# Kernel tuning notes

Measured on AMD Instinct MI355X. Metric: run time of the kernel, lower is better.

## Reference

```python
import jax, jax.numpy as jnp
import numpy as np

HIDDEN = 1024
STATE = 256
EXP = 4
LN_EPS = 1e-5


def setup_inputs() -> dict:
    key = jax.random.key(0)
    ks = jax.random.split(key, 10)
    B, T, H, S = 8, 2048, HIDDEN, STATE
    x = jax.random.normal(ks[0], (B, T, H), dtype=jnp.float32)
    A = jax.random.normal(ks[1], (S, S), dtype=jnp.float32) * 0.1
    Bm = jax.random.normal(ks[2], (S, H), dtype=jnp.float32) * 0.1
    C = jax.random.normal(ks[3], (H, S), dtype=jnp.float32) * 0.1
    D = jax.random.normal(ks[4], (H, H), dtype=jnp.float32) * 0.1
    ln_w = jnp.ones((H,), dtype=jnp.float32)
    ln_b = jnp.zeros((H,), dtype=jnp.float32)
    lim1 = 1.0 / np.sqrt(H)
    lim2 = 1.0 / np.sqrt(H * EXP)
    W1 = jax.random.uniform(ks[5], (H * EXP, H), minval=-lim1, maxval=lim1, dtype=jnp.float32)
    b1 = jax.random.uniform(ks[6], (H * EXP,), minval=-lim1, maxval=lim1, dtype=jnp.float32)
    W2 = jax.random.uniform(ks[7], (H, H * EXP), minval=-lim2, maxval=lim2, dtype=jnp.float32)
    b2 = jax.random.uniform(ks[8], (H,), minval=-lim2, maxval=lim2, dtype=jnp.float32)
    return {"x": x, "A": A, "Bm": Bm, "C": C, "D": D,
            "ln_w": ln_w, "ln_b": ln_b, "W1": W1, "b1": b1, "W2": W2, "b2": b2}


def _layernorm(y, w, b):
    mu = jnp.mean(y, axis=-1, keepdims=True)
    var = jnp.var(y, axis=-1, keepdims=True)
    return (y - mu) * jax.lax.rsqrt(var + LN_EPS) * w + b


def reference(x, A, Bm, C, D, ln_w, ln_b, W1, b1, W2, b2):
    Bsz, T, H = x.shape
    S = A.shape[0]
    state0 = jnp.zeros((Bsz, S), dtype=x.dtype)
    # Precompute input projections for all timesteps (big GEMMs outside the scan)
    xB = jnp.einsum('bth,sh->tbs', x, Bm)   # [T,B,S]
    xD = jnp.einsum('bth,oh->tbo', x, D)    # [T,B,H]

    def step(state, inp):
        xb_t, xd_t = inp
        state = jnp.tanh(state @ A.T + xb_t)
        out = state @ C.T + xd_t
        return state, out

    final_state, outs = jax.lax.scan(step, state0, (xB, xD))
    out_seq = jnp.transpose(outs, (1, 0, 2))  # [B,T,H]
    y = _layernorm(out_seq + x, ln_w, ln_b)
    # FFN (dropout is identity in eval mode); torch GELU default = exact erf
    h = jax.nn.gelu(jnp.einsum('bth,fh->btf', y, W1) + b1, approximate=False)
    y = y + jnp.einsum('btf,hf->bth', h, W2) + b2
    return (y, final_state)
```

## Files before the change

### kernel.cpp

```cpp
#include <hip/hip_runtime.h>
#include <math.h>

typedef unsigned short u16;
typedef unsigned int u32;

using short8 = __attribute__((ext_vector_type(8))) short;
using f32x4  = __attribute__((ext_vector_type(4))) float;
typedef _Float16 h2_t __attribute__((ext_vector_type(2)));

typedef const __attribute__((address_space(1))) unsigned int* gas_ptr;
typedef __attribute__((address_space(3))) unsigned int* las_ptr;

__device__ __forceinline__ void load_lds16(const void* g, void* l) {
    __builtin_amdgcn_global_load_lds((gas_ptr)g, (las_ptr)l, 16, 0, 0);
}

__device__ __forceinline__ u16 bf16b(float f) {
    u32 u = __builtin_bit_cast(u32, f);
    u += 0x7fffu + ((u >> 16) & 1u);
    return (u16)(u >> 16);
}
__device__ __forceinline__ float b2f(u16 h) {
    u32 u = (u32)h << 16;
    return __builtin_bit_cast(float, u);
}

__global__ void cvt_kernel(const float4* __restrict__ s, ushort4* __restrict__ d, int n4) {
    for (int i = blockIdx.x * blockDim.x + threadIdx.x; i < n4; i += gridDim.x * blockDim.x) {
        float4 v = s[i];
        ushort4 o;
        o.x = bf16b(v.x); o.y = bf16b(v.y); o.z = bf16b(v.z); o.w = bf16b(v.w);
        d[i] = o;
    }
}
__global__ void cvt_str_kernel(const float4* __restrict__ s, u16* __restrict__ d,
                               int K4, int n4, int stride, int col0) {
    for (int i = blockIdx.x * blockDim.x + threadIdx.x; i < n4; i += gridDim.x * blockDim.x) {
        float4 v = s[i];
        int r = i / K4, k4 = (i - r * K4) * 4;
        ushort4 o;
        o.x = bf16b(v.x); o.y = bf16b(v.y); o.z = bf16b(v.z); o.w = bf16b(v.w);
        *(ushort4*)(d + (size_t)r * stride + col0 + k4) = o;
    }
}

template<int MODE>
__global__ __launch_bounds__(256) void gemm_bf16(
    const u16* __restrict__ Ab, const u16* __restrict__ Ab2, const u16* __restrict__ Bb,
    int K, int ktiles,
    float* __restrict__ out32, u16* __restrict__ out16,
    const float* __restrict__ bias, const float* __restrict__ addf,
    const u16* __restrict__ add16, int out_stride)
{
    __shared__ __align__(16) u16 Als[128 * 64];
    __shared__ __align__(16) u16 Bls[128 * 64];

    const int tid  = threadIdx.x;
    const int lane = tid & 63;
    const int w    = tid >> 6;
    const int wr   = (w >> 1) * 64;
    const int wc   = (w & 1) * 64;
    const int fr   = lane & 15;
    const int fkB  = (lane >> 4) * 16;

    const size_t rbB = (size_t)K * 2;
    const int arow = blockIdx.y * 128 + (tid >> 3);
    const char* Ag  = (const char*)Ab + (size_t)arow * ((MODE == 1) ? 512 : rbB) + (size_t)(tid & 7) * 16;
    const char* Ag2 = (MODE == 1) ? ((const char*)Ab2 + (size_t)arow * 2048 + (size_t)(tid & 7) * 16) : nullptr;
    const char* Bg  = (const char*)Bb + ((size_t)blockIdx.x * 128 + (tid >> 3)) * rbB + (size_t)(tid & 7) * 16;
    char* Ald = (char*)Als + tid * 16;
    char* Bld = (char*)Bls + tid * 16;

    f32x4 acc[4][4];
#pragma unroll
    for (int m = 0; m < 4; ++m)
#pragma unroll
        for (int n = 0; n < 4; ++n)
            acc[m][n] = f32x4{0.f, 0.f, 0.f, 0.f};

    for (int kt = 0; kt < ktiles; ++kt) {
        __syncthreads();
        const char* Asrc;
        size_t rbA;
        if (MODE == 1) {
            if (kt < 4) { Asrc = Ag  + (size_t)kt * 128;       rbA = 512;  }
            else        { Asrc = Ag2 + (size_t)(kt - 4) * 128; rbA = 2048; }
        } else {
            Asrc = Ag + (size_t)kt * 128; rbA = rbB;
        }
        const char* Bsrc = Bg + (size_t)kt * 128;
#pragma unroll
        for (int i = 0; i < 4; ++i) {
            load_lds16(Asrc + (size_t)(i * 32) * rbA, Ald + i * 4096);
            load_lds16(Bsrc + (size_t)(i * 32) * rbB, Bld + i * 4096);
        }
        __syncthreads();
#pragma unroll
        for (int kk = 0; kk < 2; ++kk) {
            short8 af[4], bfr[4];
#pragma unroll
            for (int m = 0; m < 4; ++m)
                af[m] = *(const short8*)((const char*)Als + (wr + m * 16 + fr) * 128 + kk * 64 + fkB);
#pragma unroll
            for (int n = 0; n < 4; ++n)
                bfr[n] = *(const short8*)((const char*)Bls + (wc + n * 16 + fr) * 128 + kk * 64 + fkB);
#pragma unroll
            for (int m = 0; m < 4; ++m)
#pragma unroll
                for (int n = 0; n < 4; ++n)
                    acc[m][n] = __builtin_amdgcn_mfma_f32_16x16x32_bf16(af[m], bfr[n], acc[m][n], 0, 0, 0);
        }
    }

    const int rbase = blockIdx.y * 128 + wr + (lane >> 4) * 4;
    const int cbase = blockIdx.x * 128 + wc + fr;
#pragma unroll
    for (int m = 0; m < 4; ++m) {
#pragma unroll
        for (int n = 0; n < 4; ++n) {
            const int col = cbase + n * 16;
#pragma unroll
            for (int r = 0; r < 4; ++r) {
                const int row = rbase + m * 16 + r;
                float v = acc[m][n][r];
                if (MODE == 0) {
                    out16[(size_t)row * out_stride + col] = bf16b(v);
                } else if (MODE == 1) {
                    out16[(size_t)row * 1024 + col] = bf16b(v + addf[(size_t)row * 1024 + col]);
                } else if (MODE == 2) {
                    float u = v + bias[col];
                    u = 0.5f * u * (1.0f + erff(u * 0.70710678118654752f));
                    out16[(size_t)row * out_stride + col] = bf16b(u);
                } else {
                    out32[(size_t)row * 1024 + col] =
                        v + bias[col] + b2f(add16[(size_t)row * 1024 + col]);
                }
            }
        }
    }
}

__global__ __launch_bounds__(1024) void scan_kernel(
    const float* __restrict__ Am, const u16* __restrict__ xBb ,
    u16* __restrict__ states, float* __restrict__ fstate)
{
    __shared__ __align__(16) u32 SB[2][144];
    const int tid = threadIdx.x;
    const int b   = blockIdx.x;
    const int s   = tid >> 2;
    const int q   = tid & 3;

    h2_t a[32];
    {
        const float4* ar = (const float4*)(Am + s * 256 + q * 64);
#pragma unroll
        for (int j = 0; j < 16; ++j) {
            float4 f = ar[j];
            a[2 * j]     = h2_t{(_Float16)f.x, (_Float16)f.y};
            a[2 * j + 1] = h2_t{(_Float16)f.z, (_Float16)f.w};
        }
    }
    if (tid < 144) SB[0][tid] = 0u;

    const u16* xrow = xBb + (size_t)b * 2048 * 256 + s;
    u16* srow = states + (size_t)b * 2048 * 256 + s;
    const int widx = (s >> 6) * 72 + (s & 63);

    float xb0 = b2f(xrow[0]);
    float xb1 = b2f(xrow[256]);
    float xb2 = b2f(xrow[512]);
    float xb3 = b2f(xrow[768]);
    __syncthreads();

#define SCAN_STEP(T, XB)                                                            \
    {                                                                               \
        const u32* sp = SB[(T) & 1] + q * 36;                                       \
        float ac0 = 0.f, ac1 = 0.f, ac2 = 0.f, ac3 = 0.f;                           \
        _Pragma("unroll")                                                           \
        for (int j = 0; j < 8; ++j) {                                               \
            uint4 sv = *(const uint4*)(sp + 4 * j);                                 \
            ac0 = __builtin_amdgcn_fdot2(a[4 * j + 0], __builtin_bit_cast(h2_t, sv.x), ac0, false); \
            ac1 = __builtin_amdgcn_fdot2(a[4 * j + 1], __builtin_bit_cast(h2_t, sv.y), ac1, false); \
            ac2 = __builtin_amdgcn_fdot2(a[4 * j + 2], __builtin_bit_cast(h2_t, sv.z), ac2, false); \
            ac3 = __builtin_amdgcn_fdot2(a[4 * j + 3], __builtin_bit_cast(h2_t, sv.w), ac3, false); \
        }                                                                           \
        float zq = (ac0 + ac1) + (ac2 + ac3);                                       \
        zq += __shfl_xor(zq, 1);                                                    \
        float z = zq + __shfl_xor(zq, 2) + (XB);                                    \
        int tp = (T) + 4 <= 2047 ? (T) + 4 : 2047;                                  \
        (XB) = b2f(xrow[(size_t)tp * 256]);                                        \
        float e = __expf(2.f * z);                                                  \
        float h = 1.f - 2.f / (e + 1.f);                                            \
        if (!q) {                                                                   \
            reinterpret_cast<_Float16*>(SB[((T) + 1) & 1])[widx] = (_Float16)h;     \
            srow[(size_t)(T) * 256] = bf16b(h);                                     \
            if ((T) == 2047) fstate[b * 256 + s] = h;                               \
        }                                                                           \
        __syncthreads();                                                            \
    }

    for (int t = 0; t < 2048; t += 4) {
        SCAN_STEP(t + 0, xb0);
        SCAN_STEP(t + 1, xb1);
        SCAN_STEP(t + 2, xb2);
        SCAN_STEP(t + 3, xb3);
    }
#undef SCAN_STEP
}

__global__ __launch_bounds__(256) void ln_kernel(
    const u16* __restrict__ pre , const float* __restrict__ gam,
    const float* __restrict__ bet, u16* __restrict__ ybf)
{
    const int row = blockIdx.x, tid = threadIdx.x;
    const ushort4 pv = *(const ushort4*)(pre + (size_t)row * 1024 + tid * 4);
    float vx = b2f(pv.x), vy = b2f(pv.y), vz = b2f(pv.z), vw = b2f(pv.w);
    float sum = vx + vy + vz + vw;
    float sq  = vx * vx + vy * vy + vz * vz + vw * vw;
#pragma unroll
    for (int o = 32; o; o >>= 1) { sum += __shfl_xor(sum, o); sq += __shfl_xor(sq, o); }
    __shared__ float red[8];
    const int lane = tid & 63, wv = tid >> 6;
    if (!lane) { red[wv] = sum; red[4 + wv] = sq; }
    __syncthreads();
    sum = red[0] + red[1] + red[2] + red[3];
    sq  = red[4] + red[5] + red[6] + red[7];
    const float mu  = sum * (1.f / 1024.f);
    const float var = sq * (1.f / 1024.f) - mu * mu;
    const float rs  = rsqrtf(var + 1e-5f);
    const float4 g  = *(const float4*)(gam + tid * 4);
    const float4 be = *(const float4*)(bet + tid * 4);
    ushort4 ob;
    ob.x = bf16b((vx - mu) * rs * g.x + be.x);
    ob.y = bf16b((vy - mu) * rs * g.y + be.y);
    ob.z = bf16b((vz - mu) * rs * g.z + be.z);
    ob.w = bf16b((vw - mu) * rs * g.w + be.w);
    *(ushort4*)(ybf + (size_t)row * 1024 + tid * 4) = ob;
}

extern "C" void kernel_launch(void* const* d_in, const int* in_sizes, int n_in,
                              void* d_out, int out_size, void* d_ws, size_t ws_size,
                              hipStream_t stream)
{
    const float* x    = (const float*)d_in[0];
    const float* A    = (const float*)d_in[1];
    const float* Bm   = (const float*)d_in[2];
    const float* C    = (const float*)d_in[3];
    const float* D    = (const float*)d_in[4];
    const float* ln_w = (const float*)d_in[5];
    const float* ln_b = (const float*)d_in[6];
    const float* W1   = (const float*)d_in[7];
    const float* b1   = (const float*)d_in[8];
    const float* W2   = (const float*)d_in[9];
    const float* b2   = (const float*)d_in[10];

    char* ws = (char*)d_ws;
    u16* Bm_bf  = (u16*)(ws + 0);
    u16* CD_bf  = (u16*)(ws + 524288);
    u16* W1b    = (u16*)(ws + 3145728);
    u16* W2b    = (u16*)(ws + 11534336);
    u16* xB_bf  = (u16*)(ws + 19922944);
    u16* st_bf  = (u16*)(ws + 28311552);
    u16* y_bf   = (u16*)(ws + 36700160);
    u16* pre_bf = (u16*)(ws + 70254592);
    u16* xh_bf  = (u16*)(ws + 103809024);

    float* out = (float*)d_out;

    cvt_kernel<<<2048, 256, 0, stream>>>((const float4*)x,  (ushort4*)xh_bf, 4194304);
    cvt_kernel<<<256,  256, 0, stream>>>((const float4*)Bm, (ushort4*)Bm_bf, 65536);
    cvt_str_kernel<<<256,  256, 0, stream>>>((const float4*)C, CD_bf, 64, 65536, 1280, 0);
    cvt_str_kernel<<<1024, 256, 0, stream>>>((const float4*)D, CD_bf, 256, 262144, 1280, 256);
    cvt_kernel<<<2048, 256, 0, stream>>>((const float4*)W1, (ushort4*)W1b, 1048576);
    cvt_kernel<<<2048, 256, 0, stream>>>((const float4*)W2, (ushort4*)W2b, 1048576);

    dim3 blk(256);
    gemm_bf16<0><<<dim3(2, 128), blk, 0, stream>>>(xh_bf, nullptr, Bm_bf, 1024, 16,
        nullptr, xB_bf, nullptr, nullptr, nullptr, 256);
    scan_kernel<<<8, 1024, 0, stream>>>(A, xB_bf, st_bf, out + 16777216);
    gemm_bf16<1><<<dim3(8, 128), blk, 0, stream>>>(st_bf, xh_bf, CD_bf, 1280, 20,
        nullptr, pre_bf, nullptr, x, nullptr, 1024);
    ln_kernel<<<16384, 256, 0, stream>>>(pre_bf, ln_w, ln_b, y_bf);
    for (int c = 0; c < 4; ++c) {
        const u16* yc = y_bf + (size_t)c * 4096 * 1024;
        float* oc = out + (size_t)c * 4096 * 1024;
        gemm_bf16<2><<<dim3(32, 32), blk, 0, stream>>>(yc, nullptr, W1b, 1024, 16,
            nullptr, xh_bf, b1, nullptr, nullptr, 4096);
        gemm_bf16<3><<<dim3(8, 32), blk, 0, stream>>>(xh_bf, nullptr, W2b, 4096, 64,
            oc, nullptr, b2, nullptr, yc, 1024);
    }
}
```

Baseline: 2.221 ms.

## Restructure scan to 512 threads with 4 rows per thread group and DPP reductions

```diff
diff --git a/kernel.cpp b/kernel.cpp
--- a/kernel.cpp
+++ b/kernel.cpp
@@ -23,6 +23,12 @@
 __device__ __forceinline__ float b2f(u16 h) {
     u32 u = (u32)h << 16;
     return __builtin_bit_cast(float, u);
+}
+
+template<int CTRL>
+__device__ __forceinline__ float dpp_add(float v) {
+    int m = __builtin_amdgcn_update_dpp(0, __builtin_bit_cast(int, v), CTRL, 0xF, 0xF, true);
+    return v + __builtin_bit_cast(float, m);
 }
 
 __global__ void cvt_kernel(const float4* __restrict__ s, ushort4* __restrict__ d, int n4) {
@@ -140,72 +146,106 @@
     }
 }
 
-__global__ __launch_bounds__(1024) void scan_kernel(
+__global__ __launch_bounds__(512) void scan_kernel(
     const float* __restrict__ Am, const u16* __restrict__ xBb ,
     u16* __restrict__ states, float* __restrict__ fstate)
 {
-    __shared__ __align__(16) u32 SB[2][144];
+    __shared__ __align__(16) u32 SB[2][160];
     const int tid = threadIdx.x;
     const int b   = blockIdx.x;
-    const int s   = tid >> 2;
-    const int q   = tid & 3;
-
-    h2_t a[32];
-    {
-        const float4* ar = (const float4*)(Am + s * 256 + q * 64);
-#pragma unroll
-        for (int j = 0; j < 16; ++j) {
-            float4 f = ar[j];
-            a[2 * j]     = h2_t{(_Float16)f.x, (_Float16)f.y};
-            a[2 * j + 1] = h2_t{(_Float16)f.z, (_Float16)f.w};
-        }
-    }
-    if (tid < 144) SB[0][tid] = 0u;
-
-    const u16* xrow = xBb + (size_t)b * 2048 * 256 + s;
-    u16* srow = states + (size_t)b * 2048 * 256 + s;
-    const int widx = (s >> 6) * 72 + (s & 63);
-
-    float xb0 = b2f(xrow[0]);
-    float xb1 = b2f(xrow[256]);
-    float xb2 = b2f(xrow[512]);
-    float xb3 = b2f(xrow[768]);
+    const int g   = tid >> 3;
+    const int q   = tid & 7;
+    const int lq  = q & 3;
+
+    h2_t a[4][16];
+#pragma unroll
+    for (int r = 0; r < 4; ++r) {
+        const float4* ar = (const float4*)(Am + (size_t)(4 * g + r) * 256 + 32 * q);
+#pragma unroll
+        for (int jj = 0; jj < 8; ++jj) {
+            float4 f = ar[jj];
+            a[r][2 * jj]     = h2_t{(_Float16)f.x, (_Float16)f.y};
+            a[r][2 * jj + 1] = h2_t{(_Float16)f.z, (_Float16)f.w};
+        }
+    }
+    if (tid < 160) SB[0][tid] = 0u;
+
+    const int srw = 4 * g + lq;
+    const u16* xrow = xBb + (size_t)b * 2048 * 256 + 4 * g;
+    u16* srow = states + (size_t)b * 2048 * 256 + srw;
+    const int lbyte = (srw >> 5) * 80 + (srw & 31) * 2;
+    const bool wlane = (q < 4);
+    _Float16* sb0 = (_Float16*)((char*)&SB[0][0] + lbyte);
+    _Float16* sb1 = (_Float16*)((char*)&SB[1][0] + lbyte);
+
+    uint2 xp0 = *(const uint2*)(xrow);
+    uint2 xp1 = *(const uint2*)(xrow + 256);
+    uint2 xp2 = *(const uint2*)(xrow + 512);
+    uint2 xp3 = *(const uint2*)(xrow + 768);
     __syncthreads();
 
-#define SCAN_STEP(T, XB)                                                            \
-    {                                                                               \
-        const u32* sp = SB[(T) & 1] + q * 36;                                       \
-        float ac0 = 0.f, ac1 = 0.f, ac2 = 0.f, ac3 = 0.f;                           \
-        _Pragma("unroll")                                                           \
-        for (int j = 0; j < 8; ++j) {                                               \
-            uint4 sv = *(const uint4*)(sp + 4 * j);                                 \
-            ac0 = __builtin_amdgcn_fdot2(a[4 * j + 0], __builtin_bit_cast(h2_t, sv.x), ac0, false); \
-            ac1 = __builtin_amdgcn_fdot2(a[4 * j + 1], __builtin_bit_cast(h2_t, sv.y), ac1, false); \
-            ac2 = __builtin_amdgcn_fdot2(a[4 * j + 2], __builtin_bit_cast(h2_t, sv.z), ac2, false); \
-            ac3 = __builtin_amdgcn_fdot2(a[4 * j + 3], __builtin_bit_cast(h2_t, sv.w), ac3, false); \
-        }                                                                           \
-        float zq = (ac0 + ac1) + (ac2 + ac3);                                       \
-        zq += __shfl_xor(zq, 1);                                                    \
-        float z = zq + __shfl_xor(zq, 2) + (XB);                                    \
-        int tp = (T) + 4 <= 2047 ? (T) + 4 : 2047;                                  \
-        (XB) = b2f(xrow[(size_t)tp * 256]);                                        \
-        float e = __expf(2.f * z);                                                  \
-        float h = 1.f - 2.f / (e + 1.f);                                            \
-        if (!q) {                                                                   \
-            reinterpret_cast<_Float16*>(SB[((T) + 1) & 1])[widx] = (_Float16)h;     \
-            srow[(size_t)(T) * 256] = bf16b(h);                                     \
-            if ((T) == 2047) fstate[b * 256 + s] = h;                               \
-        }                                                                           \
-        __syncthreads();                                                            \
+#define ROW_DOT(ZR, R, W0, W1, W2, W3)                                               \
+    ZR = __builtin_amdgcn_fdot2(a[R][0],  __builtin_bit_cast(h2_t, W0.x), ZR, false); \
+    ZR = __builtin_amdgcn_fdot2(a[R][1],  __builtin_bit_cast(h2_t, W0.y), ZR, false); \
+    ZR = __builtin_amdgcn_fdot2(a[R][2],  __builtin_bit_cast(h2_t, W0.z), ZR, false); \
+    ZR = __builtin_amdgcn_fdot2(a[R][3],  __builtin_bit_cast(h2_t, W0.w), ZR, false); \
+    ZR = __builtin_amdgcn_fdot2(a[R][4],  __builtin_bit_cast(h2_t, W1.x), ZR, false); \
+    ZR = __builtin_amdgcn_fdot2(a[R][5],  __builtin_bit_cast(h2_t, W1.y), ZR, false); \
+    ZR = __builtin_amdgcn_fdot2(a[R][6],  __builtin_bit_cast(h2_t, W1.z), ZR, false); \
+    ZR = __builtin_amdgcn_fdot2(a[R][7],  __builtin_bit_cast(h2_t, W1.w), ZR, false); \
+    ZR = __builtin_amdgcn_fdot2(a[R][8],  __builtin_bit_cast(h2_t, W2.x), ZR, false); \
+    ZR = __builtin_amdgcn_fdot2(a[R][9],  __builtin_bit_cast(h2_t, W2.y), ZR, false); \
+    ZR = __builtin_amdgcn_fdot2(a[R][10], __builtin_bit_cast(h2_t, W2.z), ZR, false); \
+    ZR = __builtin_amdgcn_fdot2(a[R][11], __builtin_bit_cast(h2_t, W2.w), ZR, false); \
+    ZR = __builtin_amdgcn_fdot2(a[R][12], __builtin_bit_cast(h2_t, W3.x), ZR, false); \
+    ZR = __builtin_amdgcn_fdot2(a[R][13], __builtin_bit_cast(h2_t, W3.y), ZR, false); \
+    ZR = __builtin_amdgcn_fdot2(a[R][14], __builtin_bit_cast(h2_t, W3.z), ZR, false); \
+    ZR = __builtin_amdgcn_fdot2(a[R][15], __builtin_bit_cast(h2_t, W3.w), ZR, false);
+
+#define SCAN_STEP(T, XP)                                                             \
+    {                                                                                \
+        const u32* sp = &SB[(T) & 1][q * 20];                                        \
+        uint4 s0 = *(const uint4*)(sp + 0);                                          \
+        uint4 s1 = *(const uint4*)(sp + 4);                                          \
+        uint4 s2 = *(const uint4*)(sp + 8);                                          \
+        uint4 s3 = *(const uint4*)(sp + 12);                                         \
+        float z0 = 0.f, z1 = 0.f, z2 = 0.f, z3 = 0.f;                                \
+        ROW_DOT(z0, 0, s0, s1, s2, s3)                                               \
+        ROW_DOT(z1, 1, s0, s1, s2, s3)                                               \
+        ROW_DOT(z2, 2, s0, s1, s2, s3)                                               \
+        ROW_DOT(z3, 3, s0, s1, s2, s3)                                               \
+        z0 = dpp_add<0xB1>(z0);  z1 = dpp_add<0xB1>(z1);                             \
+        z2 = dpp_add<0xB1>(z2);  z3 = dpp_add<0xB1>(z3);                             \
+        z0 = dpp_add<0x4E>(z0);  z1 = dpp_add<0x4E>(z1);                             \
+        z2 = dpp_add<0x4E>(z2);  z3 = dpp_add<0x4E>(z3);                             \
+        z0 = dpp_add<0x141>(z0); z1 = dpp_add<0x141>(z1);                            \
+        z2 = dpp_add<0x141>(z2); z3 = dpp_add<0x141>(z3);                            \
+        float t0 = (lq & 1) ? z1 : z0;                                               \
+        float t1 = (lq & 1) ? z3 : z2;                                               \
+        float zm = (lq & 2) ? t1 : t0;                                               \
+        u32 wsel = (lq & 2) ? XP.y : XP.x;                                           \
+        u32 hsel = (lq & 1) ? (wsel >> 16) : (wsel & 0xFFFFu);                       \
+        zm += b2f((u16)hsel);                                                        \
+        int tp = (T) + 4 <= 2047 ? (T) + 4 : 2047;                                   \
+        XP = *(const uint2*)(xrow + (size_t)tp * 256);                               \
+        float e = __expf(2.f * zm);                                                  \
+        float h = 1.f - 2.f * __builtin_amdgcn_rcpf(e + 1.f);                        \
+        if (wlane) {                                                                 \
+            *((((T) + 1) & 1) ? sb1 : sb0) = (_Float16)h;                            \
+            srow[(size_t)(T) * 256] = bf16b(h);                                      \
+            if ((T) == 2047) fstate[b * 256 + srw] = h;                              \
+        }                                                                            \
+        __syncthreads();                                                             \
     }
 
     for (int t = 0; t < 2048; t += 4) {
-        SCAN_STEP(t + 0, xb0);
-        SCAN_STEP(t + 1, xb1);
-        SCAN_STEP(t + 2, xb2);
-        SCAN_STEP(t + 3, xb3);
+        SCAN_STEP(t + 0, xp0);
+        SCAN_STEP(t + 1, xp1);
+        SCAN_STEP(t + 2, xp2);
+        SCAN_STEP(t + 3, xp3);
     }
 #undef SCAN_STEP
+#undef ROW_DOT
 }
 
 __global__ __launch_bounds__(256) void ln_kernel(
@@ -277,7 +317,7 @@
     dim3 blk(256);
     gemm_bf16<0><<<dim3(2, 128), blk, 0, stream>>>(xh_bf, nullptr, Bm_bf, 1024, 16,
         nullptr, xB_bf, nullptr, nullptr, nullptr, 256);
-    scan_kernel<<<8, 1024, 0, stream>>>(A, xB_bf, st_bf, out + 16777216);
+    scan_kernel<<<8, 512, 0, stream>>>(A, xB_bf, st_bf, out + 16777216);
     gemm_bf16<1><<<dim3(8, 128), blk, 0, stream>>>(st_bf, xh_bf, CD_bf, 1280, 20,
         nullptr, pre_bf, nullptr, x, nullptr, 1024);
     ln_kernel<<<16384, 256, 0, stream>>>(pre_bf, ln_w, ln_b, y_bf);
```

Result: faster. 1.853 ms (-16.6%).

## Run recurrent scan as a single-block MFMA kernel with fp16 state

Applied to the files above, without the earlier changes.

```diff
diff --git a/kernel.cpp b/kernel.cpp
--- a/kernel.cpp
+++ b/kernel.cpp
@@ -7,6 +7,7 @@
 using short8 = __attribute__((ext_vector_type(8))) short;
 using f32x4  = __attribute__((ext_vector_type(4))) float;
 typedef _Float16 h2_t __attribute__((ext_vector_type(2)));
+using half8  = __attribute__((ext_vector_type(8))) _Float16;
 
 typedef const __attribute__((address_space(1))) unsigned int* gas_ptr;
 typedef __attribute__((address_space(3))) unsigned int* las_ptr;
@@ -23,6 +24,11 @@
 __device__ __forceinline__ float b2f(u16 h) {
     u32 u = (u32)h << 16;
     return __builtin_bit_cast(float, u);
+}
+
+__device__ __forceinline__ float tanhf_fast(float z) {
+    float e = __expf(2.0f * z);
+    return 1.0f - 2.0f * __builtin_amdgcn_rcpf(e + 1.0f);
 }
 
 __global__ void cvt_kernel(const float4* __restrict__ s, ushort4* __restrict__ d, int n4) {
@@ -33,13 +39,21 @@
         d[i] = o;
     }
 }
+template<bool F16>
 __global__ void cvt_str_kernel(const float4* __restrict__ s, u16* __restrict__ d,
                                int K4, int n4, int stride, int col0) {
     for (int i = blockIdx.x * blockDim.x + threadIdx.x; i < n4; i += gridDim.x * blockDim.x) {
         float4 v = s[i];
         int r = i / K4, k4 = (i - r * K4) * 4;
         ushort4 o;
-        o.x = bf16b(v.x); o.y = bf16b(v.y); o.z = bf16b(v.z); o.w = bf16b(v.w);
+        if (F16) {
+            o.x = __builtin_bit_cast(u16, (_Float16)v.x);
+            o.y = __builtin_bit_cast(u16, (_Float16)v.y);
+            o.z = __builtin_bit_cast(u16, (_Float16)v.z);
+            o.w = __builtin_bit_cast(u16, (_Float16)v.w);
+        } else {
+            o.x = bf16b(v.x); o.y = bf16b(v.y); o.z = bf16b(v.z); o.w = bf16b(v.w);
+        }
         *(ushort4*)(d + (size_t)r * stride + col0 + k4) = o;
     }
 }
@@ -95,6 +109,7 @@
             load_lds16(Bsrc + (size_t)(i * 32) * rbB, Bld + i * 4096);
         }
         __syncthreads();
+        const bool f16t = (MODE == 1) && (kt < 4);
 #pragma unroll
         for (int kk = 0; kk < 2; ++kk) {
             short8 af[4], bfr[4];
@@ -104,11 +119,21 @@
 #pragma unroll
             for (int n = 0; n < 4; ++n)
                 bfr[n] = *(const short8*)((const char*)Bls + (wc + n * 16 + fr) * 128 + kk * 64 + fkB);
-#pragma unroll
-            for (int m = 0; m < 4; ++m)
-#pragma unroll
-                for (int n = 0; n < 4; ++n)
-                    acc[m][n] = __builtin_amdgcn_mfma_f32_16x16x32_bf16(af[m], bfr[n], acc[m][n], 0, 0, 0);
+            if (f16t) {
+#pragma unroll
+                for (int m = 0; m < 4; ++m)
+#pragma unroll
+                    for (int n = 0; n < 4; ++n)
+                        acc[m][n] = __builtin_amdgcn_mfma_f32_16x16x32_f16(
+                            __builtin_bit_cast(half8, af[m]), __builtin_bit_cast(half8, bfr[n]),
+                            acc[m][n], 0, 0, 0);
+            } else {
+#pragma unroll
+                for (int m = 0; m < 4; ++m)
+#pragma unroll
+                    for (int n = 0; n < 4; ++n)
+                        acc[m][n] = __builtin_amdgcn_mfma_f32_16x16x32_bf16(af[m], bfr[n], acc[m][n], 0, 0, 0);
+            }
         }
     }
 
@@ -124,7 +149,7 @@
                 const int row = rbase + m * 16 + r;
                 float v = acc[m][n][r];
                 if (MODE == 0) {
-                    out16[(size_t)row * out_stride + col] = bf16b(v);
+                    out16[(size_t)row * out_stride + col] = __builtin_bit_cast(u16, (_Float16)v);
                 } else if (MODE == 1) {
                     out16[(size_t)row * 1024 + col] = bf16b(v + addf[(size_t)row * 1024 + col]);
                 } else if (MODE == 2) {
@@ -140,72 +165,117 @@
     }
 }
 
-__global__ __launch_bounds__(1024) void scan_kernel(
-    const float* __restrict__ Am, const u16* __restrict__ xBb ,
-    u16* __restrict__ states, float* __restrict__ fstate)
+__global__ __launch_bounds__(256) void scan_mfma_kernel(
+    const float* __restrict__ Am, const u16* __restrict__ xBh ,
+    u16* __restrict__ sth , float* __restrict__ fstate)
 {
-    __shared__ __align__(16) u32 SB[2][144];
+    __shared__ __align__(16) char SB[2][8192];
     const int tid = threadIdx.x;
-    const int b   = blockIdx.x;
-    const int s   = tid >> 2;
-    const int q   = tid & 3;
-
-    h2_t a[32];
+    const int l = tid & 63, w = tid >> 6;
+    const int b = l & 15, g = l >> 4;
+    const int bc = b < 8 ? b : 7;
+    const bool breal = (b < 8);
+
+    half8 af[4][8];
+#pragma unroll
+    for (int nt = 0; nt < 4; ++nt)
+#pragma unroll
+        for (int kk = 0; kk < 8; ++kk) {
+            const float* ap = Am + (size_t)(64 * w + nt * 16 + b) * 256 + kk * 32 + g * 8;
+            float4 f0 = *(const float4*)ap;
+            float4 f1 = *(const float4*)(ap + 4);
+            half8 h;
+            h[0] = (_Float16)f0.x; h[1] = (_Float16)f0.y; h[2] = (_Float16)f0.z; h[3] = (_Float16)f0.w;
+            h[4] = (_Float16)f1.x; h[5] = (_Float16)f1.y; h[6] = (_Float16)f1.z; h[7] = (_Float16)f1.w;
+            af[nt][kk] = h;
+        }
+
     {
-        const float4* ar = (const float4*)(Am + s * 256 + q * 64);
-#pragma unroll
-        for (int j = 0; j < 16; ++j) {
-            float4 f = ar[j];
-            a[2 * j]     = h2_t{(_Float16)f.x, (_Float16)f.y};
-            a[2 * j + 1] = h2_t{(_Float16)f.z, (_Float16)f.w};
-        }
-    }
-    if (tid < 144) SB[0][tid] = 0u;
-
-    const u16* xrow = xBb + (size_t)b * 2048 * 256 + s;
-    u16* srow = states + (size_t)b * 2048 * 256 + s;
-    const int widx = (s >> 6) * 72 + (s & 63);
-
-    float xb0 = b2f(xrow[0]);
-    float xb1 = b2f(xrow[256]);
-    float xb2 = b2f(xrow[512]);
-    float xb3 = b2f(xrow[768]);
+        uint4 z = uint4{0u, 0u, 0u, 0u};
+#pragma unroll
+        for (int i = 0; i < 4; ++i)
+            ((uint4*)SB)[tid + 256 * i] = z;
+    }
+
+    int n0[4], wb[4];
+    const u16* xp[4];
+    u16* sp[4];
+#pragma unroll
+    for (int nt = 0; nt < 4; ++nt) {
+        int n = 64 * w + nt * 16 + g * 4;
+        n0[nt] = n;
+        wb[nt] = (n >> 5) * 1024 + (b + 16 * ((n & 31) >> 3)) * 16 + (n & 7) * 2;
+        xp[nt] = xBh + (size_t)bc * 2048 * 256 + n;
+        sp[nt] = sth + (size_t)bc * 2048 * 256 + n;
+    }
+
+    uint2 xc0, xc1, xc2, xc3, xn0, xn1, xn2, xn3;
+    xc0 = *(const uint2*)(xp[0]); xp[0] += 256;
+    xc1 = *(const uint2*)(xp[1]); xp[1] += 256;
+    xc2 = *(const uint2*)(xp[2]); xp[2] += 256;
+    xc3 = *(const uint2*)(xp[3]); xp[3] += 256;
+    xn0 = xc0; xn1 = xc1; xn2 = xc2; xn3 = xc3;
     __syncthreads();
 
-#define SCAN_STEP(T, XB)                                                            \
-    {                                                                               \
-        const u32* sp = SB[(T) & 1] + q * 36;                                       \
-        float ac0 = 0.f, ac1 = 0.f, ac2 = 0.f, ac3 = 0.f;                           \
-        _Pragma("unroll")                                                           \
-        for (int j = 0; j < 8; ++j) {                                               \
-            uint4 sv = *(const uint4*)(sp + 4 * j);                                 \
-            ac0 = __builtin_amdgcn_fdot2(a[4 * j + 0], __builtin_bit_cast(h2_t, sv.x), ac0, false); \
-            ac1 = __builtin_amdgcn_fdot2(a[4 * j + 1], __builtin_bit_cast(h2_t, sv.y), ac1, false); \
-            ac2 = __builtin_amdgcn_fdot2(a[4 * j + 2], __builtin_bit_cast(h2_t, sv.z), ac2, false); \
-            ac3 = __builtin_amdgcn_fdot2(a[4 * j + 3], __builtin_bit_cast(h2_t, sv.w), ac3, false); \
-        }                                                                           \
-        float zq = (ac0 + ac1) + (ac2 + ac3);                                       \
-        zq += __shfl_xor(zq, 1);                                                    \
-        float z = zq + __shfl_xor(zq, 2) + (XB);                                    \
-        int tp = (T) + 4 <= 2047 ? (T) + 4 : 2047;                                  \
-        (XB) = b2f(xrow[(size_t)tp * 256]);                                        \
-        float e = __expf(2.f * z);                                                  \
-        float h = 1.f - 2.f / (e + 1.f);                                            \
-        if (!q) {                                                                   \
-            reinterpret_cast<_Float16*>(SB[((T) + 1) & 1])[widx] = (_Float16)h;     \
-            srow[(size_t)(T) * 256] = bf16b(h);                                     \
-            if ((T) == 2047) fstate[b * 256 + s] = h;                               \
-        }                                                                           \
-        __syncthreads();                                                            \
-    }
-
-    for (int t = 0; t < 2048; t += 4) {
-        SCAN_STEP(t + 0, xb0);
-        SCAN_STEP(t + 1, xb1);
-        SCAN_STEP(t + 2, xb2);
-        SCAN_STEP(t + 3, xb3);
-    }
-#undef SCAN_STEP
+#define UNPK(XC) f32x4{ (float)__builtin_bit_cast(h2_t, (XC).x)[0],            \
+                        (float)__builtin_bit_cast(h2_t, (XC).x)[1],            \
+                        (float)__builtin_bit_cast(h2_t, (XC).y)[0],            \
+                        (float)__builtin_bit_cast(h2_t, (XC).y)[1] }
+
+#define MM(KK)                                                                 \
+    acc0 = __builtin_amdgcn_mfma_f32_16x16x32_f16(af[0][KK], __builtin_bit_cast(half8, s##KK), acc0, 0, 0, 0); \
+    acc1 = __builtin_amdgcn_mfma_f32_16x16x32_f16(af[1][KK], __builtin_bit_cast(half8, s##KK), acc1, 0, 0, 0); \
+    acc2 = __builtin_amdgcn_mfma_f32_16x16x32_f16(af[2][KK], __builtin_bit_cast(half8, s##KK), acc2, 0, 0, 0); \
+    acc3 = __builtin_amdgcn_mfma_f32_16x16x32_f16(af[3][KK], __builtin_bit_cast(half8, s##KK), acc3, 0, 0, 0);
+
+#define FIN(NT, ACC, T, PW)                                                    \
+    {                                                                          \
+        float h0 = tanhf_fast((ACC)[0]);                                       \
+        float h1 = tanhf_fast((ACC)[1]);                                       \
+        float h2 = tanhf_fast((ACC)[2]);                                       \
+        float h3 = tanhf_fast((ACC)[3]);                                       \
+        h2_t pa{(_Float16)h0, (_Float16)h1};                                   \
+        h2_t pb{(_Float16)h2, (_Float16)h3};                                   \
+        uint2 pk;                                                              \
+        pk.x = __builtin_bit_cast(u32, pa);                                    \
+        pk.y = __builtin_bit_cast(u32, pb);                                    \
+        *(uint2*)(&SB[PW][0] + wb[NT]) = pk;                                   \
+        if (breal) *(uint2*)(sp[NT]) = pk;                                     \
+        sp[NT] += 256;                                                         \
+        if ((T) == 2047 && breal)                                              \
+            *(float4*)(fstate + b * 256 + n0[NT]) = float4{h0, h1, h2, h3};    \
+    }
+
+#define STEP(T, PR, PW, XC0, XC1, XC2, XC3, XN0, XN1, XN2, XN3)                \
+    {                                                                          \
+        const char* rb = &SB[PR][0] + l * 16;                                  \
+        uint4 s0 = *(const uint4*)(rb + 0 * 1024);                             \
+        uint4 s1 = *(const uint4*)(rb + 1 * 1024);                             \
+        uint4 s2 = *(const uint4*)(rb + 2 * 1024);                             \
+        uint4 s3 = *(const uint4*)(rb + 3 * 1024);                             \
+        uint4 s4 = *(const uint4*)(rb + 4 * 1024);                             \
+        uint4 s5 = *(const uint4*)(rb + 5 * 1024);                             \
+        uint4 s6 = *(const uint4*)(rb + 6 * 1024);                             \
+        uint4 s7 = *(const uint4*)(rb + 7 * 1024);                             \
+        XN0 = *(const uint2*)(xp[0]); xp[0] += 256;                            \
+        XN1 = *(const uint2*)(xp[1]); xp[1] += 256;                            \
+        XN2 = *(const uint2*)(xp[2]); xp[2] += 256;                            \
+        XN3 = *(const uint2*)(xp[3]); xp[3] += 256;                            \
+        f32x4 acc0 = UNPK(XC0), acc1 = UNPK(XC1), acc2 = UNPK(XC2), acc3 = UNPK(XC3); \
+        MM(0) MM(1) MM(2) MM(3) MM(4) MM(5) MM(6) MM(7)                        \
+        FIN(0, acc0, T, PW) FIN(1, acc1, T, PW)                                \
+        FIN(2, acc2, T, PW) FIN(3, acc3, T, PW)                                \
+        asm volatile("s_waitcnt lgkmcnt(0)\n\ts_barrier" ::: "memory");        \
+    }
+
+    for (int t = 0; t < 2048; t += 2) {
+        STEP(t,     0, 1, xc0, xc1, xc2, xc3, xn0, xn1, xn2, xn3);
+        STEP(t + 1, 1, 0, xn0, xn1, xn2, xn3, xc0, xc1, xc2, xc3);
+    }
+#undef STEP
+#undef FIN
+#undef MM
+#undef UNPK
 }
 
 __global__ __launch_bounds__(256) void ln_kernel(
@@ -259,8 +329,8 @@
     u16* CD_bf  = (u16*)(ws + 524288);
     u16* W1b    = (u16*)(ws + 3145728);
     u16* W2b    = (u16*)(ws + 11534336);
-    u16* xB_bf  = (u16*)(ws + 19922944);
-    u16* st_bf  = (u16*)(ws + 28311552);
+    u16* xB_h   = (u16*)(ws + 19922944);
+    u16* st_h   = (u16*)(ws + 28311552);
     u16* y_bf   = (u16*)(ws + 36700160);
     u16* pre_bf = (u16*)(ws + 70254592);
     u16* xh_bf  = (u16*)(ws + 103809024);
@@ -269,16 +339,16 @@
 
     cvt_kernel<<<2048, 256, 0, stream>>>((const float4*)x,  (ushort4*)xh_bf, 4194304);
     cvt_kernel<<<256,  256, 0, stream>>>((const float4*)Bm, (ushort4*)Bm_bf, 65536);
-    cvt_str_kernel<<<256,  256, 0, stream>>>((const float4*)C, CD_bf, 64, 65536, 1280, 0);
-    cvt_str_kernel<<<1024, 256, 0, stream>>>((const float4*)D, CD_bf, 256, 262144, 1280, 256);
+    cvt_str_kernel<true ><<<256,  256, 0, stream>>>((const float4*)C, CD_bf, 64, 65536, 1280, 0);
+    cvt_str_kernel<false><<<1024, 256, 0, stream>>>((const float4*)D, CD_bf, 256, 262144, 1280, 256);
     cvt_kernel<<<2048, 256, 0, stream>>>((const float4*)W1, (ushort4*)W1b, 1048576);
     cvt_kernel<<<2048, 256, 0, stream>>>((const float4*)W2, (ushort4*)W2b, 1048576);
 
     dim3 blk(256);
     gemm_bf16<0><<<dim3(2, 128), blk, 0, stream>>>(xh_bf, nullptr, Bm_bf, 1024, 16,
-        nullptr, xB_bf, nullptr, nullptr, nullptr, 256);
-    scan_kernel<<<8, 1024, 0, stream>>>(A, xB_bf, st_bf, out + 16777216);
-    gemm_bf16<1><<<dim3(8, 128), blk, 0, stream>>>(st_bf, xh_bf, CD_bf, 1280, 20,
+        nullptr, xB_h, nullptr, nullptr, nullptr, 256);
+    scan_mfma_kernel<<<1, 256, 0, stream>>>(A, xB_h, st_h, out + 16777216);
+    gemm_bf16<1><<<dim3(8, 128), blk, 0, stream>>>(st_h, xh_bf, CD_bf, 1280, 20,
         nullptr, pre_bf, nullptr, x, nullptr, 1024);
     ln_kernel<<<16384, 256, 0, stream>>>(pre_bf, ln_w, ln_b, y_bf);
     for (int c = 0; c < 4; ++c) {
```

Result: slower. 2.619 ms (+17.9%).
